# Optimization experiments

Measured on AMD Instinct MI355X. Metric: run time of the kernel, lower is better.

## Reference

```python
import jax, jax.numpy as jnp
import numpy as np
from jax import lax

T_DATA = 20000
E_NO = 2000
I_NO = 500
SUB_NO = 16
SYN_B = 3
HID = 256
T_SYN = 200
T_ENC = 80


def _causal_conv(x, kern):
    # x: [T, S] per-subunit drive; kern: [S, K] causal kernels (index = lag)
    S, K = kern.shape
    lhs = jnp.pad(x.T, ((0, 0), (K - 1, 0)))[None]        # [1, S, T+K-1]
    rhs = kern[:, ::-1][:, None, :]                        # flip then correlate == torch conv1d path
    out = lax.conv_general_dilated(lhs, rhs, (1,), 'VALID', feature_group_count=S)
    return out[0].T                                        # [T, S]


def setup_inputs() -> dict:
    key = jax.random.key(0)
    ks = jax.random.split(key, 16)
    V_in = jax.random.normal(ks[0], (T_DATA,), jnp.float32) * 5.0 - 69.0
    S_e = jax.random.bernoulli(ks[1], 0.02, (T_DATA, E_NO)).astype(jnp.float32)
    S_i = jax.random.bernoulli(ks[2], 0.02, (T_DATA, I_NO)).astype(jnp.float32)
    # synapse -> subunit one-hot assignment matrices [sub_no, n_syn]
    C_syn_e = jax.nn.one_hot(jax.random.randint(ks[3], (E_NO,), 0, SUB_NO), SUB_NO, dtype=jnp.float32).T
    C_syn_i = jax.nn.one_hot(jax.random.randint(ks[4], (I_NO,), 0, SUB_NO), SUB_NO, dtype=jnp.float32).T
    # parameters, initialized exactly as in __init__
    K_syn = jnp.stack([jnp.full((SUB_NO, SYN_B), 0.04),
                       jnp.full((SUB_NO, SYN_B), -0.02),
                       jnp.full((SUB_NO, SYN_B), 0.02)], axis=-1)          # [sub, B, 3]
    tau_syn = jnp.tile((jnp.arange(SYN_B, dtype=jnp.float32) + 1.6)[:, None], (1, 3))  # [B, 3]
    delta_syn = jnp.full((SUB_NO, 2), 2.0, jnp.float32)
    enc_bias = jnp.zeros((SUB_NO - 1,), jnp.float32)
    W_in = 2 * T_ENC - 1

    def lin(k, fan_out, fan_in):
        kw, kb = jax.random.split(k)
        s = 1.0 / np.sqrt(fan_in)
        return (jax.random.uniform(kw, (fan_out, fan_in), jnp.float32, -s, s),
                jax.random.uniform(kb, (fan_out,), jnp.float32, -s, s))

    W1, b1 = lin(ks[5], HID, W_in)
    W2, b2 = lin(ks[6], HID, HID)
    W3, b3 = lin(ks[7], HID, HID)
    W4, b4 = lin(ks[8], SUB_NO - 1, HID)
    a1 = jnp.float32(0.25)
    a2 = jnp.float32(0.25)
    a3 = jnp.float32(0.25)
    return dict(V_in=V_in, S_e=S_e, S_i=S_i, C_syn_e=C_syn_e, C_syn_i=C_syn_i,
                K_syn=K_syn, tau_syn=tau_syn, delta_syn=delta_syn, enc_bias=enc_bias,
                W1=W1, b1=b1, a1=a1, W2=W2, b2=b2, a2=a2, W3=W3, b3=b3, a3=a3,
                W4=W4, b4=b4)


def reference(V_in, S_e, S_i, C_syn_e, C_syn_i, K_syn, tau_syn, delta_syn, enc_bias,
              W1, b1, a1, W2, b2, a2, W3, b3, a3, W4, b4):
    T = V_in.shape[0]
    # ---- spike_convolve, fully vectorized over (subunit, basis) ----
    t = jnp.arange(T_SYN, dtype=V_in.dtype)                 # [T_syn]
    d = jnp.exp(delta_syn)                                   # [sub, 2]
    te = jnp.maximum(t[None, :] - d[:, 0:1], 0.0)            # [sub, T_syn]
    ti = jnp.maximum(t[None, :] - d[:, 1:2], 0.0)
    tau = jnp.exp(tau_syn)                                   # [B, 3]
    tte = te[:, None, :] / tau[None, :, 0, None]             # [sub, B, T_syn]
    tti = ti[:, None, :] / tau[None, :, 1, None]
    ker_e = jnp.einsum('sbt,sb->st', tte * jnp.exp(-tte), K_syn[:, :, 0])
    ker_i = jnp.einsum('sbt,sb->st', tti * jnp.exp(-tti), K_syn[:, :, 1])
    in_e = S_e @ C_syn_e.T                                   # [T, sub]
    in_i = S_i @ C_syn_i.T
    S_conv = _causal_conv(in_e, ker_e) + _causal_conv(in_i, ker_i)   # [T, sub]
    # ---- encode: batched sliding-window MLP (replaces per-timestep loop) ----
    W = 2 * T_ENC - 1
    Vpad = jnp.zeros((T + W,), V_in.dtype).at[T_ENC - 1:T_ENC - 1 + T].set(V_in)
    idx = jnp.arange(T)[:, None] + jnp.arange(W)[None, :]    # [T, W]
    win = Vpad[idx]                                          # [T, W]
    prelu = lambda x, a: jnp.where(x >= 0, x, a * x)
    h = prelu(win @ W1.T + b1, a1)
    h = prelu(h @ W2.T + b2, a2)
    h = prelu(h @ W3.T + b3, a3)
    nn_out = h @ W4.T + b4                                   # [T, sub-1]
    return jax.nn.sigmoid(nn_out + S_conv[:, 1:] + enc_bias)
```

## Files before the change

kernel.cpp:

```cpp
#include <hip/hip_runtime.h>
#include <cstdint>
#include <cstddef>

#define T_DATA 20000
#define E_NO 2000
#define I_NO 500
#define SUB_NO 16
#define HID 256
#define T_SYN 200
#define T_ENC 80
#define W_IN 159

typedef __attribute__((ext_vector_type(8))) __bf16 bf16x8;
typedef __attribute__((ext_vector_type(8))) short short8;
typedef __attribute__((ext_vector_type(4))) float floatx4;
typedef __attribute__((ext_vector_type(4))) unsigned int uint4v;
typedef __attribute__((ext_vector_type(2))) unsigned int uint2v;

__device__ __forceinline__ float bf2f(unsigned short u) {
    union { unsigned int i; float f; } v; v.i = ((unsigned int)u) << 16; return v.f;
}
__device__ __forceinline__ unsigned short f2bf(float f) {
    union { float f; unsigned int i; } v; v.f = f;
    unsigned int r = v.i + 0x7FFFu + ((v.i >> 16) & 1u);
    return (unsigned short)(r >> 16);
}
__device__ __forceinline__ float inload(const void* p, int i, int isbf) {
    return isbf ? bf2f(((const unsigned short*)p)[i]) : ((const float*)p)[i];
}

__device__ __forceinline__ int detect_bf(const void* Se, int* sfl) {
    if (threadIdx.x == 0) *sfl = 0;
    __syncthreads();
    const unsigned int* w = (const unsigned int*)Se;
    int la = 0;
    #pragma unroll
    for (int i = 0; i < 4; i++)
        la |= (w[i * 256 + threadIdx.x] & 0xFFFFu) ? 1 : 0;
    if (la) atomicOr(sfl, 1);
    __syncthreads();
    return *sfl;
}

#define OFF_KERE   16u
#define OFF_KERI   12816u
#define OFF_SHE    25616u
#define OFF_SHI    33616u
#define OFF_W1H    35616u
#define OFF_W1L    117536u
#define OFF_W2H    199456u
#define OFF_W2L    330528u
#define OFF_W3H    461600u
#define OFF_W3L    592672u
#define OFF_W4H    723744u
#define OFF_W4L    731424u
#define OFF_INE    739104u
#define OFF_INI    1059104u

__global__ void k_tables(const void* Se, const void* Ksyn, const void* tau_syn, const void* dly,
                         const void* Ce, const void* Ci,
                         float* ker_e, float* ker_i, unsigned char* sh_e, unsigned char* sh_i) {
    __shared__ int sfl;
    int f = detect_bf(Se, &sfl);
    int id = blockIdx.x * 256 + threadIdx.x;
    if (id < 6400) {
        int c = id < 3200 ? 0 : 1;
        int q = id - c * 3200;
        int s = q / 200, j = q - s * 200;
        float d = expf(inload(dly, s * 2 + c, f));
        float tt = fmaxf((float)j - d, 0.0f);
        float acc = 0.f;
        #pragma unroll
        for (int b = 0; b < 3; b++) {
            float tau = expf(inload(tau_syn, b * 3 + c, f));
            float x = tt / tau;
            acc += x * expf(-x) * inload(Ksyn, (s * 3 + b) * 3 + c, f);
        }
        (c == 0 ? ker_e : ker_i)[s * 200 + j] = acc;
    } else if (id < 8400) {
        int e = id - 6400;
        int a = 0;
        for (int s = 0; s < 16; s++) if (inload(Ce, s * E_NO + e, f) > 0.5f) a = s;
        sh_e[e] = (unsigned char)(a * 8);
    } else if (id < 8900) {
        int e = id - 8400;
        int a = 0;
        for (int s = 0; s < 16; s++) if (inload(Ci, s * I_NO + e, f) > 0.5f) a = s;
        sh_i[e] = (unsigned char)(a * 8);
    }
}

__device__ __forceinline__ void acc_slot(unsigned int b, unsigned int sh,
                                         unsigned long long& lo, unsigned long long& hi) {
    unsigned int up = sh >> 6;
    unsigned int s6 = sh & 63;
    lo += (unsigned long long)(b & (up ^ 1u)) << s6;
    hi += (unsigned long long)(b & up) << s6;
}

__global__ void __launch_bounds__(256) k_spikes(const void* Se, const void* Si,
                         const unsigned char* sh_e, const unsigned char* sh_i,
                         const void* W1, const void* W2, const void* W3, const void* W4,
                         unsigned char* in_e, unsigned char* in_i,
                         unsigned short* W1h, unsigned short* W1l,
                         unsigned short* W2h, unsigned short* W2l,
                         unsigned short* W3h, unsigned short* W3l,
                         unsigned short* W4h, unsigned short* W4l) {
    __shared__ int sfl;
    __shared__ __align__(8) unsigned char she[E_NO];
    __shared__ __align__(8) unsigned char shi[I_NO];
    for (int i = threadIdx.x; i < E_NO / 4; i += 256)
        ((unsigned int*)she)[i] = ((const unsigned int*)sh_e)[i];
    for (int i = threadIdx.x; i < I_NO / 4; i += 256)
        ((unsigned int*)shi)[i] = ((const unsigned int*)sh_i)[i];
    int f = detect_bf(Se, &sfl);
    int lane = threadIdx.x & 63;
    int wave = threadIdx.x >> 6;
    int t = blockIdx.x * 4 + wave;
    unsigned long long e0 = 0, e1 = 0, i0 = 0, i1 = 0;
    if (f) {
        const uint4v* re = (const uint4v*)((const unsigned short*)Se + (size_t)t * E_NO);
        #pragma unroll
        for (int it = 0; it < 4; it++) {
            int c = it * 64 + lane;
            if (c < 250) {
                uint4v v = re[c];
                unsigned long long q = *(const unsigned long long*)&she[c * 8];
                #pragma unroll
                for (int w = 0; w < 4; w++) {
                    unsigned int x = v[w];
                    acc_slot((x >> 7) & 1u,  (unsigned int)(q >> (16 * w)) & 0xFFu, e0, e1);
                    acc_slot((x >> 23) & 1u, (unsigned int)(q >> (16 * w + 8)) & 0xFFu, e0, e1);
                }
            }
        }
        const uint2v* ri = (const uint2v*)((const unsigned short*)Si + (size_t)t * I_NO);
        #pragma unroll
        for (int it = 0; it < 2; it++) {
            int c = it * 64 + lane;
            if (c < 125) {
                uint2v v = ri[c];
                unsigned int q = *(const unsigned int*)&shi[c * 4];
                #pragma unroll
                for (int w = 0; w < 2; w++) {
                    unsigned int x = v[w];
                    acc_slot((x >> 7) & 1u,  (q >> (16 * w)) & 0xFFu, i0, i1);
                    acc_slot((x >> 23) & 1u, (q >> (16 * w + 8)) & 0xFFu, i0, i1);
                }
            }
        }
    } else {
        const uint4v* re = (const uint4v*)((const float*)Se + (size_t)t * E_NO);
        #pragma unroll
        for (int it = 0; it < 8; it++) {
            int c = it * 64 + lane;
            if (c < 500) {
                uint4v v = re[c];
                unsigned int q = *(const unsigned int*)&she[c * 4];
                #pragma unroll
                for (int w = 0; w < 4; w++)
                    acc_slot((v[w] >> 23) & 1u, (q >> (8 * w)) & 0xFFu, e0, e1);
            }
        }
        const uint2v* ri = (const uint2v*)((const float*)Si + (size_t)t * I_NO);
        #pragma unroll
        for (int it = 0; it < 4; it++) {
            int c = it * 64 + lane;
            if (c < 250) {
                uint2v v = ri[c];
                unsigned int q = *(const unsigned short*)&shi[c * 2];
                #pragma unroll
                for (int w = 0; w < 2; w++)
                    acc_slot((v[w] >> 23) & 1u, (q >> (8 * w)) & 0xFFu, i0, i1);
            }
        }
    }
    for (int off = 32; off; off >>= 1) {
        e0 += __shfl_xor(e0, off);
        e1 += __shfl_xor(e1, off);
        i0 += __shfl_xor(i0, off);
        i1 += __shfl_xor(i1, off);
    }
    if (lane < 16) {
        unsigned long long a = (lane < 8) ? e0 : e1;
        in_e[(size_t)t * 16 + lane] = (unsigned char)((a >> ((lane & 7) * 8)) & 0xFF);
    } else if (lane < 32) {
        int s = lane - 16;
        unsigned long long a = (s < 8) ? i0 : i1;
        in_i[(size_t)t * 16 + s] = (unsigned char)((a >> ((s & 7) * 8)) & 0xFF);
    }
    if (blockIdx.x < 687) {
        int q = blockIdx.x * 256 + threadIdx.x;
        if (q < 40960) {
            int n = q / 160, k = q - n * 160;
            float v = (k < W_IN) ? inload(W1, n * W_IN + k, f) : 0.f;
            unsigned short hi = f2bf(v);
            W1h[q] = hi;
            W1l[q] = f2bf(v - bf2f(hi));
        } else if (q < 106496) {
            int r = q - 40960;
            float v = inload(W2, r, f);
            unsigned short hi = f2bf(v);
            W2h[r] = hi;
            W2l[r] = f2bf(v - bf2f(hi));
        } else if (q < 172032) {
            int r = q - 106496;
            float v = inload(W3, r, f);
            unsigned short hi = f2bf(v);
            W3h[r] = hi;
            W3l[r] = f2bf(v - bf2f(hi));
        } else {
            int r = q - 172032;
            float v = inload(W4, r, f);
            unsigned short hi = f2bf(v);
            W4h[r] = hi;
            W4l[r] = f2bf(v - bf2f(hi));
        }
    }
}

template<bool BF>
__device__ __forceinline__ void mlp_body(
    const void* V,
    const unsigned short* W1h, const unsigned short* W1l, const void* b1, const void* a1p,
    const unsigned short* W2h, const unsigned short* W2l, const void* b2, const void* a2p,
    const unsigned short* W3h, const unsigned short* W3l, const void* b3, const void* a3p,
    const unsigned short* W4h, const unsigned short* W4l, const void* b4,
    const void* encb, const float* Sc, void* out,
    unsigned short* Ahi, unsigned short* Alo)
{
    int tid = threadIdx.x;
    int lane = tid & 63, wave = tid >> 6;
    int lm = lane & 15, quad = lane >> 4;
    int t0 = blockIdx.x * 64;

    auto ld = [&](const void* p, int i) -> float {
        return BF ? bf2f(((const unsigned short*)p)[i]) : ((const float*)p)[i];
    };

    for (int idx = tid; idx < 64 * 160; idx += 256) {
        int m = idx / 160, k = idx - m * 160;
        int tg = t0 + m + k - (T_ENC - 1);
        float v = 0.f;
        if (k < W_IN && tg >= 0 && tg < T_DATA) v = ld(V, tg);
        unsigned short hi = f2bf(v);
        int col = (((k >> 3) ^ (m & 31)) << 3) | (k & 7);
        Ahi[m * 256 + col] = hi;
        if (!BF) Alo[m * 256 + col] = f2bf(v - bf2f(hi));
    }
    __syncthreads();

    floatx4 acc[4][4];
    auto aoff = [&](int mt, int ks) {
        int arow = mt * 16 + lm;
        return arow * 256 + ((((ks << 2) | quad) ^ (arow & 31)) << 3);
    };

    auto epi = [&](const void* bias, float alpha) {
        __syncthreads();
        #pragma unroll
        for (int mt = 0; mt < 4; mt++) {
            #pragma unroll
            for (int nt = 0; nt < 4; nt++) {
                int cn = wave * 64 + nt * 16 + lm;
                float bb = ld(bias, cn);
                #pragma unroll
                for (int j = 0; j < 4; j++) {
                    int row = mt * 16 + quad * 4 + j;
                    float h = acc[mt][nt][j] + bb;
                    h = (h >= 0.f) ? h : alpha * h;
                    unsigned short hi = f2bf(h);
                    int col = (((cn >> 3) ^ (row & 31)) << 3) | (cn & 7);
                    Ahi[row * 256 + col] = hi;
                    if (!BF) Alo[row * 256 + col] = f2bf(h - bf2f(hi));
                }
            }
        }
        __syncthreads();
    };

    floatx4 z = {0.f, 0.f, 0.f, 0.f};
    {
        #pragma unroll
        for (int mt = 0; mt < 4; mt++)
            #pragma unroll
            for (int nt = 0; nt < 4; nt++) acc[mt][nt] = z;
        if (BF) {
            bf16x8 Bh[5][4];
            #pragma unroll
            for (int ks = 0; ks < 5; ks++)
                #pragma unroll
                for (int nt = 0; nt < 4; nt++)
                    Bh[ks][nt] = *(const bf16x8*)(W1h + (size_t)(wave * 64 + nt * 16 + lm) * 160 + ks * 32 + quad * 8);
            #pragma unroll
            for (int ks = 0; ks < 5; ks++) {
                bf16x8 a[4];
                #pragma unroll
                for (int mt = 0; mt < 4; mt++) a[mt] = *(const bf16x8*)&Ahi[aoff(mt, ks)];
                #pragma unroll
                for (int nt = 0; nt < 4; nt++)
                    #pragma unroll
                    for (int mt = 0; mt < 4; mt++)
                        acc[mt][nt] = __builtin_amdgcn_mfma_f32_16x16x32_bf16(a[mt], Bh[ks][nt], acc[mt][nt], 0, 0, 0);
            }
        } else {
            for (int ks = 0; ks < 5; ks++) {
                bf16x8 ah[4], al[4];
                #pragma unroll
                for (int mt = 0; mt < 4; mt++) {
                    ah[mt] = *(const bf16x8*)&Ahi[aoff(mt, ks)];
                    al[mt] = *(const bf16x8*)&Alo[aoff(mt, ks)];
                }
                #pragma unroll
                for (int nt = 0; nt < 4; nt++) {
                    size_t bo = (size_t)(wave * 64 + nt * 16 + lm) * 160 + ks * 32 + quad * 8;
                    bf16x8 bh = *(const bf16x8*)(W1h + bo);
                    bf16x8 bl = *(const bf16x8*)(W1l + bo);
                    #pragma unroll
                    for (int mt = 0; mt < 4; mt++) {
                        acc[mt][nt] = __builtin_amdgcn_mfma_f32_16x16x32_bf16(ah[mt], bh, acc[mt][nt], 0, 0, 0);
                        acc[mt][nt] = __builtin_amdgcn_mfma_f32_16x16x32_bf16(al[mt], bh, acc[mt][nt], 0, 0, 0);
                        acc[mt][nt] = __builtin_amdgcn_mfma_f32_16x16x32_bf16(ah[mt], bl, acc[mt][nt], 0, 0, 0);
                    }
                }
            }
        }
        epi(b1, ld(a1p, 0));
    }
    const unsigned short* Whs[2] = {W2h, W3h};
    const unsigned short* Wls[2] = {W2l, W3l};
    const void* bs[2] = {b2, b3};
    const void* as_[2] = {a2p, a3p};
    for (int l = 0; l < 2; l++) {
        #pragma unroll
        for (int mt = 0; mt < 4; mt++)
            #pragma unroll
            for (int nt = 0; nt < 4; nt++) acc[mt][nt] = z;
        const unsigned short* Wh = Whs[l];
        const unsigned short* Wl = Wls[l];
        if (BF) {
            bf16x8 Bh[8][4];
            #pragma unroll
            for (int ks = 0; ks < 8; ks++)
                #pragma unroll
                for (int nt = 0; nt < 4; nt++)
                    Bh[ks][nt] = *(const bf16x8*)(Wh + (size_t)(wave * 64 + nt * 16 + lm) * 256 + ks * 32 + quad * 8);
            #pragma unroll
            for (int ks = 0; ks < 8; ks++) {
                bf16x8 a[4];
                #pragma unroll
                for (int mt = 0; mt < 4; mt++) a[mt] = *(const bf16x8*)&Ahi[aoff(mt, ks)];
                #pragma unroll
                for (int nt = 0; nt < 4; nt++)
                    #pragma unroll
                    for (int mt = 0; mt < 4; mt++)
                        acc[mt][nt] = __builtin_amdgcn_mfma_f32_16x16x32_bf16(a[mt], Bh[ks][nt], acc[mt][nt], 0, 0, 0);
            }
        } else {
            for (int ks = 0; ks < 8; ks++) {
                bf16x8 ah[4], al[4];
                #pragma unroll
                for (int mt = 0; mt < 4; mt++) {
                    ah[mt] = *(const bf16x8*)&Ahi[aoff(mt, ks)];
                    al[mt] = *(const bf16x8*)&Alo[aoff(mt, ks)];
                }
                #pragma unroll
                for (int nt = 0; nt < 4; nt++) {
                    size_t bo = (size_t)(wave * 64 + nt * 16 + lm) * 256 + ks * 32 + quad * 8;
                    bf16x8 bh = *(const bf16x8*)(Wh + bo);
                    bf16x8 bl = *(const bf16x8*)(Wl + bo);
                    #pragma unroll
                    for (int mt = 0; mt < 4; mt++) {
                        acc[mt][nt] = __builtin_amdgcn_mfma_f32_16x16x32_bf16(ah[mt], bh, acc[mt][nt], 0, 0, 0);
                        acc[mt][nt] = __builtin_amdgcn_mfma_f32_16x16x32_bf16(al[mt], bh, acc[mt][nt], 0, 0, 0);
                        acc[mt][nt] = __builtin_amdgcn_mfma_f32_16x16x32_bf16(ah[mt], bl, acc[mt][nt], 0, 0, 0);
                    }
                }
            }
        }
        epi(bs[l], ld(as_[l], 0));
    }
    {
        int mt = wave;
        short8 z8 = {0, 0, 0, 0, 0, 0, 0, 0};
        bf16x8 bz = __builtin_bit_cast(bf16x8, z8);
        floatx4 a4 = z;
        #pragma unroll
        for (int ks = 0; ks < 8; ks++) {
            bf16x8 ah = *(const bf16x8*)&Ahi[aoff(mt, ks)];
            bf16x8 bh = bz;
            if (lm < 15)
                bh = *(const bf16x8*)(W4h + (size_t)lm * 256 + ks * 32 + quad * 8);
            a4 = __builtin_amdgcn_mfma_f32_16x16x32_bf16(ah, bh, a4, 0, 0, 0);
            if (!BF) {
                bf16x8 al = *(const bf16x8*)&Alo[aoff(mt, ks)];
                bf16x8 bl = bz;
                if (lm < 15)
                    bl = *(const bf16x8*)(W4l + (size_t)lm * 256 + ks * 32 + quad * 8);
                a4 = __builtin_amdgcn_mfma_f32_16x16x32_bf16(al, bh, a4, 0, 0, 0);
                a4 = __builtin_amdgcn_mfma_f32_16x16x32_bf16(ah, bl, a4, 0, 0, 0);
            }
        }
        if (lm < 15) {
            float bb = ld(b4, lm) + ld(encb, lm);
            #pragma unroll
            for (int j = 0; j < 4; j++) {
                int row = mt * 16 + quad * 4 + j;
                int t = t0 + row;
                if (t < T_DATA) {
                    float x = a4[j] + bb + Sc[row * 16 + lm + 1];
                    x = fminf(fmaxf(x, -40.f), 40.f);
                    float sg = 1.f / (1.f + expf(-x));
                    if (BF) ((unsigned short*)out)[(size_t)t * 15 + lm] = f2bf(sg);
                    else    ((float*)out)[(size_t)t * 15 + lm] = sg;
                }
            }
        }
    }
}

__global__ void __launch_bounds__(256, 2) k_convmlp(
    const void* Se, const void* V,
    const unsigned char* in_e, const unsigned char* in_i,
    const float* ker_e, const float* ker_i,
    const unsigned short* W1h, const unsigned short* W1l, const void* b1, const void* a1p,
    const unsigned short* W2h, const unsigned short* W2l, const void* b2, const void* a2p,
    const unsigned short* W3h, const unsigned short* W3l, const void* b3, const void* a3p,
    const unsigned short* W4h, const unsigned short* W4l, const void* b4,
    const void* encb, void* out) {
    __shared__ __align__(16) unsigned char smem[65536];
    __shared__ __align__(16) float Sc[64 * 16];
    __shared__ int sfl;

    float* se = (float*)smem;
    float* si = se + 263 * 17;
    float* ke = si + 263 * 17;
    float* ki = ke + 16 * 201;

    int t0 = blockIdx.x * 64;
    for (int idx = threadIdx.x; idx < 263 * 4; idx += 256) {
        int r = idx >> 2, wi = idx & 3;
        int t = t0 - 199 + r;
        unsigned int ve = 0, vi = 0;
        if (t >= 0 && t < T_DATA) {
            ve = ((const unsigned int*)in_e)[t * 4 + wi];
            vi = ((const unsigned int*)in_i)[t * 4 + wi];
        }
        #pragma unroll
        for (int b = 0; b < 4; b++) {
            se[r * 17 + wi * 4 + b] = (float)((ve >> (8 * b)) & 0xFF);
            si[r * 17 + wi * 4 + b] = (float)((vi >> (8 * b)) & 0xFF);
        }
    }
    for (int idx = threadIdx.x; idx < 3200; idx += 256) {
        int s2 = idx / 200, j = idx - s2 * 200;
        ke[s2 * 201 + j] = ker_e[idx];
        ki[s2 * 201 + j] = ker_i[idx];
    }
    int f = detect_bf(Se, &sfl);

    {
        int s = threadIdx.x & 15, g4 = (threadIdx.x >> 4) * 4;
        float a0 = 0.f, a1 = 0.f, a2 = 0.f, a3 = 0.f;
        float w0 = se[(g4 + 199) * 17 + s], w1 = se[(g4 + 200) * 17 + s];
        float w2 = se[(g4 + 201) * 17 + s], w3 = se[(g4 + 202) * 17 + s];
        float x0 = si[(g4 + 199) * 17 + s], x1 = si[(g4 + 200) * 17 + s];
        float x2 = si[(g4 + 201) * 17 + s], x3 = si[(g4 + 202) * 17 + s];
        #pragma unroll 4
        for (int j = 0; j < 200; j++) {
            float kej = ke[s * 201 + j];
            float kij = ki[s * 201 + j];
            a0 += w0 * kej + x0 * kij;
            a1 += w1 * kej + x1 * kij;
            a2 += w2 * kej + x2 * kij;
            a3 += w3 * kej + x3 * kij;
            int lr = g4 + 198 - j; lr = lr < 0 ? 0 : lr;
            float nw = se[lr * 17 + s], nx = si[lr * 17 + s];
            w3 = w2; w2 = w1; w1 = w0; w0 = nw;
            x3 = x2; x2 = x1; x1 = x0; x0 = nx;
        }
        Sc[(g4 + 0) * 16 + s] = a0;
        Sc[(g4 + 1) * 16 + s] = a1;
        Sc[(g4 + 2) * 16 + s] = a2;
        Sc[(g4 + 3) * 16 + s] = a3;
    }
    __syncthreads();

    unsigned short* Ahi = (unsigned short*)smem;
    unsigned short* Alo = Ahi + 64 * 256;
    if (f)
        mlp_body<true>(V, W1h, W1l, b1, a1p, W2h, W2l, b2, a2p, W3h, W3l, b3, a3p,
                       W4h, W4l, b4, encb, Sc, out, Ahi, Alo);
    else
        mlp_body<false>(V, W1h, W1l, b1, a1p, W2h, W2l, b2, a2p, W3h, W3l, b3, a3p,
                        W4h, W4l, b4, encb, Sc, out, Ahi, Alo);
}

extern "C" void kernel_launch(void* const* d_in, const int* in_sizes, int n_in,
                              void* d_out, int out_size, void* d_ws, size_t ws_size,
                              hipStream_t stream) {
    const void* V    = d_in[0];
    const void* Se   = d_in[1];
    const void* Si   = d_in[2];
    const void* Ce   = d_in[3];
    const void* Ci   = d_in[4];
    const void* Ksyn = d_in[5];
    const void* tau  = d_in[6];
    const void* dly  = d_in[7];
    const void* encb = d_in[8];
    const void* W1   = d_in[9];
    const void* b1   = d_in[10];
    const void* a1   = d_in[11];
    const void* W2   = d_in[12];
    const void* b2   = d_in[13];
    const void* a2   = d_in[14];
    const void* W3   = d_in[15];
    const void* b3   = d_in[16];
    const void* a3   = d_in[17];
    const void* W4   = d_in[18];
    const void* b4   = d_in[19];

    char* w = (char*)d_ws;
    float* ker_e = (float*)(w + OFF_KERE);
    float* ker_i = (float*)(w + OFF_KERI);
    unsigned char* sh_e = (unsigned char*)(w + OFF_SHE);
    unsigned char* sh_i = (unsigned char*)(w + OFF_SHI);
    unsigned short* W1h = (unsigned short*)(w + OFF_W1H);
    unsigned short* W1l = (unsigned short*)(w + OFF_W1L);
    unsigned short* W2h = (unsigned short*)(w + OFF_W2H);
    unsigned short* W2l = (unsigned short*)(w + OFF_W2L);
    unsigned short* W3h = (unsigned short*)(w + OFF_W3H);
    unsigned short* W3l = (unsigned short*)(w + OFF_W3L);
    unsigned short* W4h = (unsigned short*)(w + OFF_W4H);
    unsigned short* W4l = (unsigned short*)(w + OFF_W4L);
    unsigned char* in_e = (unsigned char*)(w + OFF_INE);
    unsigned char* in_i = (unsigned char*)(w + OFF_INI);

    k_tables<<<35, 256, 0, stream>>>(Se, Ksyn, tau, dly, Ce, Ci,
                                     ker_e, ker_i, sh_e, sh_i);
    k_spikes<<<5000, 256, 0, stream>>>(Se, Si, sh_e, sh_i, W1, W2, W3, W4,
                                       in_e, in_i,
                                       W1h, W1l, W2h, W2l, W3h, W3l, W4h, W4l);
    k_convmlp<<<313, 256, 0, stream>>>(Se, V, in_e, in_i, ker_e, ker_i,
                                       W1h, W1l, b1, a1, W2h, W2l, b2, a2,
                                       W3h, W3l, b3, a3, W4h, W4l, b4,
                                       encb, d_out);
}
```

Baseline: 366.4 us.

## Halve convmlp time tile to 32 rows, shrink LDS, raise occupancy

The fused conv+MLP kernel now processes 32 timesteps per block instead of 64, doubling the grid to 625 blocks. Shared memory is cut by storing the spike windows as bf16 and sizing them to the smaller tile, and launch bounds go to 3 blocks per CU. The bf16 MLP path loads weights in two halves to reduce register pressure, and the convolution reads its kernel taps as float4 vectors. The aim is better occupancy and CU fill on the 256-CU part, at the cost of loading the weights and the 199-row convolution halo twice as often per output row.

```diff
diff --git a/kernel.cpp b/kernel.cpp
--- a/kernel.cpp
+++ b/kernel.cpp
@@ -219,6 +219,9 @@
     }
 }
 
+#define CM 32
+#define NROWS 231
+
 template<bool BF>
 __device__ __forceinline__ void mlp_body(
     const void* V,
@@ -232,13 +235,13 @@
     int tid = threadIdx.x;
     int lane = tid & 63, wave = tid >> 6;
     int lm = lane & 15, quad = lane >> 4;
-    int t0 = blockIdx.x * 64;
+    int t0 = blockIdx.x * CM;
 
     auto ld = [&](const void* p, int i) -> float {
         return BF ? bf2f(((const unsigned short*)p)[i]) : ((const float*)p)[i];
     };
 
-    for (int idx = tid; idx < 64 * 160; idx += 256) {
+    for (int idx = tid; idx < CM * 160; idx += 256) {
         int m = idx / 160, k = idx - m * 160;
         int tg = t0 + m + k - (T_ENC - 1);
         float v = 0.f;
@@ -250,7 +253,7 @@
     }
     __syncthreads();
 
-    floatx4 acc[4][4];
+    floatx4 acc[2][4];
     auto aoff = [&](int mt, int ks) {
         int arow = mt * 16 + lm;
         return arow * 256 + ((((ks << 2) | quad) ^ (arow & 31)) << 3);
@@ -259,7 +262,7 @@
     auto epi = [&](const void* bias, float alpha) {
         __syncthreads();
         #pragma unroll
-        for (int mt = 0; mt < 4; mt++) {
+        for (int mt = 0; mt < 2; mt++) {
             #pragma unroll
             for (int nt = 0; nt < 4; nt++) {
                 int cn = wave * 64 + nt * 16 + lm;
@@ -282,7 +285,7 @@
     floatx4 z = {0.f, 0.f, 0.f, 0.f};
     {
         #pragma unroll
-        for (int mt = 0; mt < 4; mt++)
+        for (int mt = 0; mt < 2; mt++)
             #pragma unroll
             for (int nt = 0; nt < 4; nt++) acc[mt][nt] = z;
         if (BF) {
@@ -294,20 +297,20 @@
                     Bh[ks][nt] = *(const bf16x8*)(W1h + (size_t)(wave * 64 + nt * 16 + lm) * 160 + ks * 32 + quad * 8);
             #pragma unroll
             for (int ks = 0; ks < 5; ks++) {
-                bf16x8 a[4];
-                #pragma unroll
-                for (int mt = 0; mt < 4; mt++) a[mt] = *(const bf16x8*)&Ahi[aoff(mt, ks)];
+                bf16x8 a[2];
+                #pragma unroll
+                for (int mt = 0; mt < 2; mt++) a[mt] = *(const bf16x8*)&Ahi[aoff(mt, ks)];
                 #pragma unroll
                 for (int nt = 0; nt < 4; nt++)
                     #pragma unroll
-                    for (int mt = 0; mt < 4; mt++)
+                    for (int mt = 0; mt < 2; mt++)
                         acc[mt][nt] = __builtin_amdgcn_mfma_f32_16x16x32_bf16(a[mt], Bh[ks][nt], acc[mt][nt], 0, 0, 0);
             }
         } else {
             for (int ks = 0; ks < 5; ks++) {
-                bf16x8 ah[4], al[4];
-                #pragma unroll
-                for (int mt = 0; mt < 4; mt++) {
+                bf16x8 ah[2], al[2];
+                #pragma unroll
+                for (int mt = 0; mt < 2; mt++) {
                     ah[mt] = *(const bf16x8*)&Ahi[aoff(mt, ks)];
                     al[mt] = *(const bf16x8*)&Alo[aoff(mt, ks)];
                 }
@@ -317,7 +320,7 @@
                     bf16x8 bh = *(const bf16x8*)(W1h + bo);
                     bf16x8 bl = *(const bf16x8*)(W1l + bo);
                     #pragma unroll
-                    for (int mt = 0; mt < 4; mt++) {
+                    for (int mt = 0; mt < 2; mt++) {
                         acc[mt][nt] = __builtin_amdgcn_mfma_f32_16x16x32_bf16(ah[mt], bh, acc[mt][nt], 0, 0, 0);
                         acc[mt][nt] = __builtin_amdgcn_mfma_f32_16x16x32_bf16(al[mt], bh, acc[mt][nt], 0, 0, 0);
                         acc[mt][nt] = __builtin_amdgcn_mfma_f32_16x16x32_bf16(ah[mt], bl, acc[mt][nt], 0, 0, 0);
@@ -333,34 +336,38 @@
     const void* as_[2] = {a2p, a3p};
     for (int l = 0; l < 2; l++) {
         #pragma unroll
-        for (int mt = 0; mt < 4; mt++)
+        for (int mt = 0; mt < 2; mt++)
             #pragma unroll
             for (int nt = 0; nt < 4; nt++) acc[mt][nt] = z;
         const unsigned short* Wh = Whs[l];
         const unsigned short* Wl = Wls[l];
         if (BF) {
-            bf16x8 Bh[8][4];
-            #pragma unroll
-            for (int ks = 0; ks < 8; ks++)
-                #pragma unroll
-                for (int nt = 0; nt < 4; nt++)
-                    Bh[ks][nt] = *(const bf16x8*)(Wh + (size_t)(wave * 64 + nt * 16 + lm) * 256 + ks * 32 + quad * 8);
-            #pragma unroll
-            for (int ks = 0; ks < 8; ks++) {
-                bf16x8 a[4];
-                #pragma unroll
-                for (int mt = 0; mt < 4; mt++) a[mt] = *(const bf16x8*)&Ahi[aoff(mt, ks)];
-                #pragma unroll
-                for (int nt = 0; nt < 4; nt++)
+            #pragma unroll
+            for (int half = 0; half < 2; half++) {
+                bf16x8 Bh[4][4];
+                #pragma unroll
+                for (int c = 0; c < 4; c++)
                     #pragma unroll
-                    for (int mt = 0; mt < 4; mt++)
-                        acc[mt][nt] = __builtin_amdgcn_mfma_f32_16x16x32_bf16(a[mt], Bh[ks][nt], acc[mt][nt], 0, 0, 0);
+                    for (int nt = 0; nt < 4; nt++)
+                        Bh[c][nt] = *(const bf16x8*)(Wh + (size_t)(wave * 64 + nt * 16 + lm) * 256 + (half * 4 + c) * 32 + quad * 8);
+                #pragma unroll
+                for (int c = 0; c < 4; c++) {
+                    int ks = half * 4 + c;
+                    bf16x8 a[2];
+                    #pragma unroll
+                    for (int mt = 0; mt < 2; mt++) a[mt] = *(const bf16x8*)&Ahi[aoff(mt, ks)];
+                    #pragma unroll
+                    for (int nt = 0; nt < 4; nt++)
+                        #pragma unroll
+                        for (int mt = 0; mt < 2; mt++)
+                            acc[mt][nt] = __builtin_amdgcn_mfma_f32_16x16x32_bf16(a[mt], Bh[c][nt], acc[mt][nt], 0, 0, 0);
+                }
             }
         } else {
             for (int ks = 0; ks < 8; ks++) {
-                bf16x8 ah[4], al[4];
-                #pragma unroll
-                for (int mt = 0; mt < 4; mt++) {
+                bf16x8 ah[2], al[2];
+                #pragma unroll
+                for (int mt = 0; mt < 2; mt++) {
                     ah[mt] = *(const bf16x8*)&Ahi[aoff(mt, ks)];
                     al[mt] = *(const bf16x8*)&Alo[aoff(mt, ks)];
                 }
@@ -370,7 +377,7 @@
                     bf16x8 bh = *(const bf16x8*)(Wh + bo);
                     bf16x8 bl = *(const bf16x8*)(Wl + bo);
                     #pragma unroll
-                    for (int mt = 0; mt < 4; mt++) {
+                    for (int mt = 0; mt < 2; mt++) {
                         acc[mt][nt] = __builtin_amdgcn_mfma_f32_16x16x32_bf16(ah[mt], bh, acc[mt][nt], 0, 0, 0);
                         acc[mt][nt] = __builtin_amdgcn_mfma_f32_16x16x32_bf16(al[mt], bh, acc[mt][nt], 0, 0, 0);
                         acc[mt][nt] = __builtin_amdgcn_mfma_f32_16x16x32_bf16(ah[mt], bl, acc[mt][nt], 0, 0, 0);
@@ -380,7 +387,7 @@
         }
         epi(bs[l], ld(as_[l], 0));
     }
-    {
+    if (wave < 2) {
         int mt = wave;
         short8 z8 = {0, 0, 0, 0, 0, 0, 0, 0};
         bf16x8 bz = __builtin_bit_cast(bf16x8, z8);
@@ -419,7 +426,7 @@
     }
 }
 
-__global__ void __launch_bounds__(256, 2) k_convmlp(
+__global__ void __launch_bounds__(256, 3) k_convmlp(
     const void* Se, const void* V,
     const unsigned char* in_e, const unsigned char* in_i,
     const float* ker_e, const float* ker_i,
@@ -428,17 +435,17 @@
     const unsigned short* W3h, const unsigned short* W3l, const void* b3, const void* a3p,
     const unsigned short* W4h, const unsigned short* W4l, const void* b4,
     const void* encb, void* out) {
-    __shared__ __align__(16) unsigned char smem[65536];
-    __shared__ __align__(16) float Sc[64 * 16];
+    __shared__ __align__(16) unsigned char smem[41856];
+    __shared__ __align__(16) float Sc[CM * 16];
     __shared__ int sfl;
 
-    float* se = (float*)smem;
-    float* si = se + 263 * 17;
-    float* ke = si + 263 * 17;
-    float* ki = ke + 16 * 201;
-
-    int t0 = blockIdx.x * 64;
-    for (int idx = threadIdx.x; idx < 263 * 4; idx += 256) {
+    unsigned short* se16 = (unsigned short*)smem;
+    unsigned short* si16 = se16 + NROWS * 17;
+    float* kef = (float*)(smem + 15712);
+    float* kif = kef + 16 * 204;
+
+    int t0 = blockIdx.x * CM;
+    for (int idx = threadIdx.x; idx < NROWS * 4; idx += 256) {
         int r = idx >> 2, wi = idx & 3;
         int t = t0 - 199 + r;
         unsigned int ve = 0, vi = 0;
@@ -448,36 +455,39 @@
         }
         #pragma unroll
         for (int b = 0; b < 4; b++) {
-            se[r * 17 + wi * 4 + b] = (float)((ve >> (8 * b)) & 0xFF);
-            si[r * 17 + wi * 4 + b] = (float)((vi >> (8 * b)) & 0xFF);
+            se16[r * 17 + wi * 4 + b] = f2bf((float)((ve >> (8 * b)) & 0xFF));
+            si16[r * 17 + wi * 4 + b] = f2bf((float)((vi >> (8 * b)) & 0xFF));
         }
     }
     for (int idx = threadIdx.x; idx < 3200; idx += 256) {
         int s2 = idx / 200, j = idx - s2 * 200;
-        ke[s2 * 201 + j] = ker_e[idx];
-        ki[s2 * 201 + j] = ker_i[idx];
+        kef[s2 * 204 + j] = ker_e[idx];
+        kif[s2 * 204 + j] = ker_i[idx];
     }
     int f = detect_bf(Se, &sfl);
 
-    {
+    if (threadIdx.x < 128) {
         int s = threadIdx.x & 15, g4 = (threadIdx.x >> 4) * 4;
         float a0 = 0.f, a1 = 0.f, a2 = 0.f, a3 = 0.f;
-        float w0 = se[(g4 + 199) * 17 + s], w1 = se[(g4 + 200) * 17 + s];
-        float w2 = se[(g4 + 201) * 17 + s], w3 = se[(g4 + 202) * 17 + s];
-        float x0 = si[(g4 + 199) * 17 + s], x1 = si[(g4 + 200) * 17 + s];
-        float x2 = si[(g4 + 201) * 17 + s], x3 = si[(g4 + 202) * 17 + s];
-        #pragma unroll 4
-        for (int j = 0; j < 200; j++) {
-            float kej = ke[s * 201 + j];
-            float kij = ki[s * 201 + j];
-            a0 += w0 * kej + x0 * kij;
-            a1 += w1 * kej + x1 * kij;
-            a2 += w2 * kej + x2 * kij;
-            a3 += w3 * kej + x3 * kij;
-            int lr = g4 + 198 - j; lr = lr < 0 ? 0 : lr;
-            float nw = se[lr * 17 + s], nx = si[lr * 17 + s];
-            w3 = w2; w2 = w1; w1 = w0; w0 = nw;
-            x3 = x2; x2 = x1; x1 = x0; x0 = nx;
+        float w0 = bf2f(se16[(g4 + 199) * 17 + s]), w1 = bf2f(se16[(g4 + 200) * 17 + s]);
+        float w2 = bf2f(se16[(g4 + 201) * 17 + s]), w3 = bf2f(se16[(g4 + 202) * 17 + s]);
+        float x0 = bf2f(si16[(g4 + 199) * 17 + s]), x1 = bf2f(si16[(g4 + 200) * 17 + s]);
+        float x2 = bf2f(si16[(g4 + 201) * 17 + s]), x3 = bf2f(si16[(g4 + 202) * 17 + s]);
+        for (int j = 0; j < 200; j += 4) {
+            floatx4 ke4 = *(const floatx4*)&kef[s * 204 + j];
+            floatx4 ki4 = *(const floatx4*)&kif[s * 204 + j];
+            #pragma unroll
+            for (int q = 0; q < 4; q++) {
+                float kej = ke4[q], kij = ki4[q];
+                a0 += w0 * kej + x0 * kij;
+                a1 += w1 * kej + x1 * kij;
+                a2 += w2 * kej + x2 * kij;
+                a3 += w3 * kej + x3 * kij;
+                int lr = g4 + 198 - j - q; lr = lr < 0 ? 0 : lr;
+                float nw = bf2f(se16[lr * 17 + s]), nx = bf2f(si16[lr * 17 + s]);
+                w3 = w2; w2 = w1; w1 = w0; w0 = nw;
+                x3 = x2; x2 = x1; x1 = x0; x0 = nx;
+            }
         }
         Sc[(g4 + 0) * 16 + s] = a0;
         Sc[(g4 + 1) * 16 + s] = a1;
@@ -487,7 +497,7 @@
     __syncthreads();
 
     unsigned short* Ahi = (unsigned short*)smem;
-    unsigned short* Alo = Ahi + 64 * 256;
+    unsigned short* Alo = Ahi + CM * 256;
     if (f)
         mlp_body<true>(V, W1h, W1l, b1, a1p, W2h, W2l, b2, a2p, W3h, W3l, b3, a3p,
                        W4h, W4l, b4, encb, Sc, out, Ahi, Alo);
@@ -541,7 +551,7 @@
     k_spikes<<<5000, 256, 0, stream>>>(Se, Si, sh_e, sh_i, W1, W2, W3, W4,
                                        in_e, in_i,
                                        W1h, W1l, W2h, W2l, W3h, W3l, W4h, W4l);
-    k_convmlp<<<313, 256, 0, stream>>>(Se, V, in_e, in_i, ker_e, ker_i,
+    k_convmlp<<<625, 256, 0, stream>>>(Se, V, in_e, in_i, ker_e, ker_i,
                                        W1h, W1l, b1, a1, W2h, W2l, b2, a2,
                                        W3h, W3l, b3, a3, W4h, W4l, b4,
                                        encb, d_out);
```

Result: slower. 374.6 us (+2.2%).

## Pre-swizzle MLP weights into MFMA fragment order and prefetch W1 before conv

Applied to the files above, without the earlier changes.

The weight-prep kernel now stores W1..W4 hi/lo bf16 copies in a per-lane MFMA fragment layout, so each wave's B loads are fully contiguous 16-byte-per-lane reads. W4 is padded to 16 rows at prep time, which removes the lane-masked loads in the final layer. The W1 hi fragments are loaded into registers at kernel start, before the convolution stage, so their global latency overlaps the conv work. The fp32 path's k-loops are also unrolled. In exchange, register pressure rises because 20 bf16x8 fragments stay live across the conv phase, which could cause spills under launch bounds of 256 threads and 2 blocks.

```diff
diff --git a/kernel.cpp b/kernel.cpp
--- a/kernel.cpp
+++ b/kernel.cpp
@@ -53,9 +53,9 @@
 #define OFF_W3H    461600u
 #define OFF_W3L    592672u
 #define OFF_W4H    723744u
-#define OFF_W4L    731424u
-#define OFF_INE    739104u
-#define OFF_INI    1059104u
+#define OFF_W4L    731936u
+#define OFF_INE    740128u
+#define OFF_INI    1060128u
 
 __global__ void k_tables(const void* Se, const void* Ksyn, const void* tau_syn, const void* dly,
                          const void* Ce, const void* Ci,
@@ -189,32 +189,46 @@
         unsigned long long a = (s < 8) ? i0 : i1;
         in_i[(size_t)t * 16 + s] = (unsigned char)((a >> ((s & 7) * 8)) & 0xFF);
     }
-    if (blockIdx.x < 687) {
+    if (blockIdx.x < 688) {
         int q = blockIdx.x * 256 + threadIdx.x;
         if (q < 40960) {
-            int n = q / 160, k = q - n * 160;
+            int j = q & 7, l = (q >> 3) & 63, r = q >> 9;
+            int ks = r % 5, tile = r / 5;
+            int n = tile * 16 + (l & 15);
+            int k = ks * 32 + (l >> 4) * 8 + j;
             float v = (k < W_IN) ? inload(W1, n * W_IN + k, f) : 0.f;
             unsigned short hi = f2bf(v);
             W1h[q] = hi;
             W1l[q] = f2bf(v - bf2f(hi));
         } else if (q < 106496) {
-            int r = q - 40960;
-            float v = inload(W2, r, f);
+            int p = q - 40960;
+            int j = p & 7, l = (p >> 3) & 63, r = p >> 9;
+            int ks = r & 7, tile = r >> 3;
+            int n = tile * 16 + (l & 15);
+            int k = ks * 32 + (l >> 4) * 8 + j;
+            float v = inload(W2, n * 256 + k, f);
             unsigned short hi = f2bf(v);
-            W2h[r] = hi;
-            W2l[r] = f2bf(v - bf2f(hi));
+            W2h[p] = hi;
+            W2l[p] = f2bf(v - bf2f(hi));
         } else if (q < 172032) {
-            int r = q - 106496;
-            float v = inload(W3, r, f);
+            int p = q - 106496;
+            int j = p & 7, l = (p >> 3) & 63, r = p >> 9;
+            int ks = r & 7, tile = r >> 3;
+            int n = tile * 16 + (l & 15);
+            int k = ks * 32 + (l >> 4) * 8 + j;
+            float v = inload(W3, n * 256 + k, f);
             unsigned short hi = f2bf(v);
-            W3h[r] = hi;
-            W3l[r] = f2bf(v - bf2f(hi));
+            W3h[p] = hi;
+            W3l[p] = f2bf(v - bf2f(hi));
         } else {
-            int r = q - 172032;
-            float v = inload(W4, r, f);
+            int p = q - 172032;
+            int j = p & 7, l = (p >> 3) & 63, ks = p >> 9;
+            int lm = l & 15, quad = l >> 4;
+            float v = 0.f;
+            if (lm < 15) v = inload(W4, lm * 256 + ks * 32 + quad * 8 + j, f);
             unsigned short hi = f2bf(v);
-            W4h[r] = hi;
-            W4l[r] = f2bf(v - bf2f(hi));
+            W4h[p] = hi;
+            W4l[p] = f2bf(v - bf2f(hi));
         }
     }
 }
@@ -227,7 +241,8 @@
     const unsigned short* W3h, const unsigned short* W3l, const void* b3, const void* a3p,
     const unsigned short* W4h, const unsigned short* W4l, const void* b4,
     const void* encb, const float* Sc, void* out,
-    unsigned short* Ahi, unsigned short* Alo)
+    unsigned short* Ahi, unsigned short* Alo,
+    const bf16x8 (&Bh1)[5][4])
 {
     int tid = threadIdx.x;
     int lane = tid & 63, wave = tid >> 6;
@@ -237,6 +252,8 @@
     auto ld = [&](const void* p, int i) -> float {
         return BF ? bf2f(((const unsigned short*)p)[i]) : ((const float*)p)[i];
     };
+    auto boff1 = [&](int ks, int nt) { return (size_t)((((wave * 4 + nt) * 5 + ks) * 64 + lane) << 3); };
+    auto boff  = [&](int ks, int nt) { return (size_t)((((wave * 4 + nt) * 8 + ks) * 64 + lane) << 3); };
 
     for (int idx = tid; idx < 64 * 160; idx += 256) {
         int m = idx / 160, k = idx - m * 160;
@@ -286,12 +303,6 @@
             #pragma unroll
             for (int nt = 0; nt < 4; nt++) acc[mt][nt] = z;
         if (BF) {
-            bf16x8 Bh[5][4];
-            #pragma unroll
-            for (int ks = 0; ks < 5; ks++)
-                #pragma unroll
-                for (int nt = 0; nt < 4; nt++)
-                    Bh[ks][nt] = *(const bf16x8*)(W1h + (size_t)(wave * 64 + nt * 16 + lm) * 160 + ks * 32 + quad * 8);
             #pragma unroll
             for (int ks = 0; ks < 5; ks++) {
                 bf16x8 a[4];
@@ -301,9 +312,10 @@
                 for (int nt = 0; nt < 4; nt++)
                     #pragma unroll
                     for (int mt = 0; mt < 4; mt++)
-                        acc[mt][nt] = __builtin_amdgcn_mfma_f32_16x16x32_bf16(a[mt], Bh[ks][nt], acc[mt][nt], 0, 0, 0);
+                        acc[mt][nt] = __builtin_amdgcn_mfma_f32_16x16x32_bf16(a[mt], Bh1[ks][nt], acc[mt][nt], 0, 0, 0);
             }
         } else {
+            #pragma unroll
             for (int ks = 0; ks < 5; ks++) {
                 bf16x8 ah[4], al[4];
                 #pragma unroll
@@ -313,9 +325,8 @@
                 }
                 #pragma unroll
                 for (int nt = 0; nt < 4; nt++) {
-                    size_t bo = (size_t)(wave * 64 + nt * 16 + lm) * 160 + ks * 32 + quad * 8;
-                    bf16x8 bh = *(const bf16x8*)(W1h + bo);
-                    bf16x8 bl = *(const bf16x8*)(W1l + bo);
+                    bf16x8 bh = Bh1[ks][nt];
+                    bf16x8 bl = *(const bf16x8*)(W1l + boff1(ks, nt));
                     #pragma unroll
                     for (int mt = 0; mt < 4; mt++) {
                         acc[mt][nt] = __builtin_amdgcn_mfma_f32_16x16x32_bf16(ah[mt], bh, acc[mt][nt], 0, 0, 0);
@@ -344,7 +355,7 @@
             for (int ks = 0; ks < 8; ks++)
                 #pragma unroll
                 for (int nt = 0; nt < 4; nt++)
-                    Bh[ks][nt] = *(const bf16x8*)(Wh + (size_t)(wave * 64 + nt * 16 + lm) * 256 + ks * 32 + quad * 8);
+                    Bh[ks][nt] = *(const bf16x8*)(Wh + boff(ks, nt));
             #pragma unroll
             for (int ks = 0; ks < 8; ks++) {
                 bf16x8 a[4];
@@ -357,6 +368,7 @@
                         acc[mt][nt] = __builtin_amdgcn_mfma_f32_16x16x32_bf16(a[mt], Bh[ks][nt], acc[mt][nt], 0, 0, 0);
             }
         } else {
+            #pragma unroll
             for (int ks = 0; ks < 8; ks++) {
                 bf16x8 ah[4], al[4];
                 #pragma unroll
@@ -366,9 +378,8 @@
                 }
                 #pragma unroll
                 for (int nt = 0; nt < 4; nt++) {
-                    size_t bo = (size_t)(wave * 64 + nt * 16 + lm) * 256 + ks * 32 + quad * 8;
-                    bf16x8 bh = *(const bf16x8*)(Wh + bo);
-                    bf16x8 bl = *(const bf16x8*)(Wl + bo);
+                    bf16x8 bh = *(const bf16x8*)(Wh + boff(ks, nt));
+                    bf16x8 bl = *(const bf16x8*)(Wl + boff(ks, nt));
                     #pragma unroll
                     for (int mt = 0; mt < 4; mt++) {
                         acc[mt][nt] = __builtin_amdgcn_mfma_f32_16x16x32_bf16(ah[mt], bh, acc[mt][nt], 0, 0, 0);
@@ -382,21 +393,15 @@
     }
     {
         int mt = wave;
-        short8 z8 = {0, 0, 0, 0, 0, 0, 0, 0};
-        bf16x8 bz = __builtin_bit_cast(bf16x8, z8);
         floatx4 a4 = z;
         #pragma unroll
         for (int ks = 0; ks < 8; ks++) {
             bf16x8 ah = *(const bf16x8*)&Ahi[aoff(mt, ks)];
-            bf16x8 bh = bz;
-            if (lm < 15)
-                bh = *(const bf16x8*)(W4h + (size_t)lm * 256 + ks * 32 + quad * 8);
+            bf16x8 bh = *(const bf16x8*)(W4h + (size_t)((ks * 64 + lane) << 3));
             a4 = __builtin_amdgcn_mfma_f32_16x16x32_bf16(ah, bh, a4, 0, 0, 0);
             if (!BF) {
                 bf16x8 al = *(const bf16x8*)&Alo[aoff(mt, ks)];
-                bf16x8 bl = bz;
-                if (lm < 15)
-                    bl = *(const bf16x8*)(W4l + (size_t)lm * 256 + ks * 32 + quad * 8);
+                bf16x8 bl = *(const bf16x8*)(W4l + (size_t)((ks * 64 + lane) << 3));
                 a4 = __builtin_amdgcn_mfma_f32_16x16x32_bf16(al, bh, a4, 0, 0, 0);
                 a4 = __builtin_amdgcn_mfma_f32_16x16x32_bf16(ah, bl, a4, 0, 0, 0);
             }
@@ -436,6 +441,15 @@
     float* si = se + 263 * 17;
     float* ke = si + 263 * 17;
     float* ki = ke + 16 * 201;
+
+    int lane = threadIdx.x & 63, wave = threadIdx.x >> 6;
+
+    bf16x8 Bh1[5][4];
+    #pragma unroll
+    for (int ks = 0; ks < 5; ks++)
+        #pragma unroll
+        for (int nt = 0; nt < 4; nt++)
+            Bh1[ks][nt] = *(const bf16x8*)(W1h + (size_t)((((wave * 4 + nt) * 5 + ks) * 64 + lane) << 3));
 
     int t0 = blockIdx.x * 64;
     for (int idx = threadIdx.x; idx < 263 * 4; idx += 256) {
@@ -490,10 +504,10 @@
     unsigned short* Alo = Ahi + 64 * 256;
     if (f)
         mlp_body<true>(V, W1h, W1l, b1, a1p, W2h, W2l, b2, a2p, W3h, W3l, b3, a3p,
-                       W4h, W4l, b4, encb, Sc, out, Ahi, Alo);
+                       W4h, W4l, b4, encb, Sc, out, Ahi, Alo, Bh1);
     else
         mlp_body<false>(V, W1h, W1l, b1, a1p, W2h, W2l, b2, a2p, W3h, W3l, b3, a3p,
-                        W4h, W4l, b4, encb, Sc, out, Ahi, Alo);
+                        W4h, W4l, b4, encb, Sc, out, Ahi, Alo, Bh1);
 }
 
 extern "C" void kernel_launch(void* const* d_in, const int* in_sizes, int n_in,
```

After: 355.4 us. 1.03x faster.
